# Optimization experiments

Measured on AMD Instinct MI355X. Metric: run time of the kernel, lower is better.

Reference implementation:

```python
import jax, jax.numpy as jnp
import numpy as np

EPS = 1e-08

def _householder(x, v):
    # x: [B,S,r], v: [B,S,r]; H x = x - 2 v_n (v_n . x), v_n = v/||v||
    v_norm_sq = jnp.sum(v * v, axis=-1, keepdims=True) + EPS
    v_n = v / jnp.sqrt(v_norm_sq)
    vTx = jnp.sum(x * v_n, axis=-1, keepdims=True)
    return x - 2.0 * v_n * vTx

def setup_inputs() -> dict:
    key = jax.random.key(0)
    ks = jax.random.split(key, 8)
    B, S, D, R = 4, 4096, 1024, 256
    N_IN, N_PROC, N_OUT, K = 16, 64, 16, 8
    x = jax.random.normal(ks[0], (B, S, D), dtype=jnp.float32)
    input_idx = jax.random.randint(ks[1], (B, S), 0, N_IN)
    process_indices = jax.random.randint(ks[2], (B, S, K), 0, N_PROC)
    output_idx = jax.random.randint(ks[3], (B, S), 0, N_OUT)
    # learned params (orthogonal-ish init approximated by scaled gaussian)
    input_neurons = jax.random.normal(ks[4], (N_IN, D, R), dtype=jnp.float32) / np.sqrt(D)
    pv = jax.random.normal(ks[5], (N_PROC, R), dtype=jnp.float32)
    process_neurons = pv / (jnp.linalg.norm(pv, axis=-1, keepdims=True) + EPS)
    output_neurons = jax.random.normal(ks[6], (N_OUT, R, D), dtype=jnp.float32) / np.sqrt(D)
    return {"x": x, "input_neurons": input_neurons, "process_neurons": process_neurons,
            "output_neurons": output_neurons, "input_idx": input_idx,
            "process_indices": process_indices, "output_idx": output_idx}

def reference(x, input_neurons, process_neurons, output_neurons,
              input_idx, process_indices, output_idx):
    # ---- input projection (hard selection): d_model -> rank ----
    # compute all-expert projections then gather per token (avoids [B,S,D,R] gather)
    all_in = jnp.einsum('bsd,ndr->bsnr', x, input_neurons)          # [B,S,n_in,R]
    h = jnp.take_along_axis(all_in, input_idx[..., None, None], axis=2)[:, :, 0, :]  # [B,S,R]
    # ---- process: k sequential Householder reflections ----
    selected_v = process_neurons[process_indices]                    # [B,S,k,R]
    vs = jnp.moveaxis(selected_v, 2, 0)                              # [k,B,S,R]
    def step(carry, v):
        return _householder(carry, v), None
    h, _ = jax.lax.scan(step, h, vs)
    # ---- output projection (hard selection): rank -> d_model ----
    all_out = jnp.einsum('bsr,nrd->bsnd', h, output_neurons)         # [B,S,n_out,D]
    out = jnp.take_along_axis(all_out, output_idx[..., None, None], axis=2)[:, :, 0, :]
    return out
```

## Files before the change

kernel.cpp:

```cpp
#include <hip/hip_runtime.h>
#include <hip/hip_bf16.h>

#define NT    16384
#define DM    1024
#define RK    256
#define N_IN  16
#define N_OUT 16
#define KHH   8
#define MAXTOK 1536
#define BM    64
#define TPE   (MAXTOK / BM)
#define KC    4

typedef short bf16x8 __attribute__((ext_vector_type(8)));
typedef float f32x4 __attribute__((ext_vector_type(4)));
typedef unsigned short u16;
typedef u16 u16x8 __attribute__((ext_vector_type(8)));
typedef u16 u16x4 __attribute__((ext_vector_type(4)));

__device__ __forceinline__ u16 f2bf(float f) {
  __hip_bfloat16 b = __float2bfloat16(f);
  return *reinterpret_cast<u16*>(&b);
}
__device__ __forceinline__ float bf2f(u16 u) {
  return __uint_as_float((unsigned)u << 16);
}

__device__ __forceinline__ void gl_lds16(const void* g, void* lds) {
  __builtin_amdgcn_global_load_lds(
      (const __attribute__((address_space(1))) void*)g,
      (__attribute__((address_space(3))) void*)lds, 16, 0, 0);
}

__global__ __launch_bounds__(256) void build_lists_pn(
    const int* __restrict__ in_idx, const int* __restrict__ out_idx,
    const float* __restrict__ pn,
    int* __restrict__ list_in, int* __restrict__ cnt_in,
    int* __restrict__ list_out, int* __restrict__ cnt_out,
    float* __restrict__ pnorm2) {
  const int b = blockIdx.x;
  const int tid = threadIdx.x, lane = tid & 63, wid = tid >> 6;

  if (b == 32) {
    const int p = tid >> 2, q = tid & 3;
    const float* row = pn + (size_t)p * RK + q * 64;
    float s = 0.f;
#pragma unroll
    for (int i = 0; i < 16; i++) {
      const float4 v = ((const float4*)row)[i];
      s += v.x * v.x + v.y * v.y + v.z * v.z + v.w * v.w;
    }
    s += __shfl_xor(s, 1);
    s += __shfl_xor(s, 2);
    if (q == 0) pnorm2[p] = s + 1e-8f;
    return;
  }

  const int e = b & 15, which = b >> 4;
  const int* __restrict__ idx = which ? out_idx : in_idx;
  int* __restrict__ list = (which ? list_out : list_in) + (size_t)e * NT;
  int* __restrict__ cnt = (which ? cnt_out : cnt_in) + e;

  __shared__ int wsum[4];
  const unsigned long long lt = (1ull << lane) - 1ull;
  int off = 0;
  for (int base = 0; base < NT; base += 1024) {
    const int4 iv = ((const int4*)(idx + base))[tid];
    const bool f0 = iv.x == e, f1 = iv.y == e, f2 = iv.z == e, f3 = iv.w == e;
    const unsigned long long m0 = __ballot(f0), m1 = __ballot(f1),
                             m2 = __ballot(f2), m3 = __ballot(f3);
    const int below = __popcll(m0 & lt) + __popcll(m1 & lt) +
                      __popcll(m2 & lt) + __popcll(m3 & lt);
    const int wtot = __popcll(m0) + __popcll(m1) + __popcll(m2) + __popcll(m3);
    if (lane == 0) wsum[wid] = wtot;
    __syncthreads();
    int b0 = 0, tot = 0;
#pragma unroll
    for (int w = 0; w < 4; w++) { if (w < wid) b0 += wsum[w]; tot += wsum[w]; }
    int pos = off + b0 + below;
    const int t = base + tid * 4;
    if (f0) list[pos++] = t;
    if (f1) list[pos++] = t + 1;
    if (f2) list[pos++] = t + 2;
    if (f3) list[pos++] = t + 3;
    off += tot;
    __syncthreads();
  }
  if (tid == 0) *cnt = off;
}

__global__ __launch_bounds__(256) void transpose_cvt2(
    const float* __restrict__ Win, const float* __restrict__ Wout,
    u16* __restrict__ WinT, u16* __restrict__ WoT) {
  const int z = blockIdx.z;
  const float* __restrict__ src = z ? Wout : Win;
  u16* __restrict__ dst = z ? WoT : WinT;
  const int R = z ? RK : DM, C = z ? DM : RK;
  const int e = blockIdx.y;
  const int tilesC = C >> 6;
  const int tr = (blockIdx.x / tilesC) << 6;
  const int tc = (blockIdx.x % tilesC) << 6;
  __shared__ float ls[64][65];
  const int t = threadIdx.x;
  const int row = t >> 2, q = t & 3;
  const float* s = src + (size_t)e * R * C + (size_t)(tr + row) * C + tc + q * 16;
#pragma unroll
  for (int j = 0; j < 4; j++) {
    const float4 v = ((const float4*)s)[j];
    ls[row][q * 16 + j * 4 + 0] = v.x;
    ls[row][q * 16 + j * 4 + 1] = v.y;
    ls[row][q * 16 + j * 4 + 2] = v.z;
    ls[row][q * 16 + j * 4 + 3] = v.w;
  }
  __syncthreads();
  const int cc = t >> 2;
  u16x8 o0, o1;
#pragma unroll
  for (int j = 0; j < 8; j++) o0[j] = f2bf(ls[q * 16 + j][cc]);
#pragma unroll
  for (int j = 0; j < 8; j++) o1[j] = f2bf(ls[q * 16 + 8 + j][cc]);
  u16* d = dst + (size_t)e * C * R + (size_t)(tc + cc) * R + tr + q * 16;
  ((u16x8*)d)[0] = o0;
  ((u16x8*)d)[1] = o1;
}

__global__ __launch_bounds__(256, 4) void input_gemm_part(
    const float* __restrict__ x, const u16* __restrict__ WinT,
    const int* __restrict__ list, const int* __restrict__ cnt,
    u16* __restrict__ h4) {
  const int bid = blockIdx.x;
  const int xcd = bid & 7;
  int j = bid >> 3;
  const int tile = j % TPE;
  j /= TPE;
  const int nb = j & 1;
  const int e = xcd * 2 + ((j >> 1) & 1);
  const int kc = j >> 2;
  const int nt = cnt[e];
  const int t0 = tile * BM;
  if (t0 >= nt) return;
  const int* __restrict__ lst = list + (size_t)e * NT + t0;
  const int ntok = min(BM, nt - t0);

  __shared__ __align__(16) u16 As[BM * 64];
  __shared__ __align__(16) u16 Bs[128 * 64];
  __shared__ int toks[BM];

  const int tid = threadIdx.x, lane = tid & 63, w = tid >> 6;
  if (tid < BM) toks[tid] = lst[tid < ntok ? tid : 0];
  __syncthreads();

  const int arow = tid >> 3, k8 = tid & 7;
  const float* axp0 = x + (size_t)toks[arow] * DM + kc * 256 + k8 * 8;
  const float* axp1 = x + (size_t)toks[arow + 32] * DM + kc * 256 + k8 * 8;
  const int aoff0 = arow * 128 + ((k8 ^ (arow & 7)) << 4);
  const int aoff1 = (arow + 32) * 128 + ((k8 ^ (arow & 7)) << 4);

  const int sub = lane >> 3;
  const int swz8 = ((lane & 7) ^ sub) * 8;
  const u16* Wbase = WinT + (size_t)e * RK * DM + (size_t)(nb * 128) * DM + kc * 256;

  f32x4 acc[4][2];
#pragma unroll
  for (int m = 0; m < 4; m++)
#pragma unroll
    for (int jx = 0; jx < 2; jx++) acc[m][jx] = (f32x4)0.f;

  const int l15 = lane & 15, lg = lane >> 4;

  float4 af[2][2][2];
#pragma unroll
  for (int p = 0; p < 2; ++p) {
    af[p][0][0] = ((const float4*)(axp0 + p * 64))[0];
    af[p][0][1] = ((const float4*)(axp0 + p * 64))[1];
    af[p][1][0] = ((const float4*)(axp1 + p * 64))[0];
    af[p][1][1] = ((const float4*)(axp1 + p * 64))[1];
  }

#pragma unroll
  for (int it = 0; it < 4; ++it) {
    const int s = it & 1;
    const int k0 = it * 64;
    if (it) __syncthreads();
    u16x8 a0, a1;
    a0[0] = f2bf(af[s][0][0].x); a0[1] = f2bf(af[s][0][0].y);
    a0[2] = f2bf(af[s][0][0].z); a0[3] = f2bf(af[s][0][0].w);
    a0[4] = f2bf(af[s][0][1].x); a0[5] = f2bf(af[s][0][1].y);
    a0[6] = f2bf(af[s][0][1].z); a0[7] = f2bf(af[s][0][1].w);
    a1[0] = f2bf(af[s][1][0].x); a1[1] = f2bf(af[s][1][0].y);
    a1[2] = f2bf(af[s][1][0].z); a1[3] = f2bf(af[s][1][0].w);
    a1[4] = f2bf(af[s][1][1].x); a1[5] = f2bf(af[s][1][1].y);
    a1[6] = f2bf(af[s][1][1].z); a1[7] = f2bf(af[s][1][1].w);
    if (it + 2 < 4) {
      af[s][0][0] = ((const float4*)(axp0 + (it + 2) * 64))[0];
      af[s][0][1] = ((const float4*)(axp0 + (it + 2) * 64))[1];
      af[s][1][0] = ((const float4*)(axp1 + (it + 2) * 64))[0];
      af[s][1][1] = ((const float4*)(axp1 + (it + 2) * 64))[1];
    }
#pragma unroll
    for (int i = 0; i < 4; ++i) {
      const int g = w * 4 + i;
      const int n = g * 8 + sub;
      gl_lds16(Wbase + (size_t)n * DM + k0 + swz8, Bs + g * 512);
    }
    *(u16x8*)((char*)As + aoff0) = a0;
    *(u16x8*)((char*)As + aoff1) = a1;
    __syncthreads();
#pragma unroll
    for (int kk = 0; kk < 2; ++kk) {
      const int sw = (((kk * 4 + lg) ^ (l15 & 7)) << 4);
      bf16x8 fa[4];
#pragma unroll
      for (int m = 0; m < 4; ++m)
        fa[m] = *(const bf16x8*)((const char*)As + (m * 16 + l15) * 128 + sw);
#pragma unroll
      for (int jx = 0; jx < 2; ++jx) {
        const int n = w * 32 + jx * 16 + l15;
        const bf16x8 fb = *(const bf16x8*)((const char*)Bs + n * 128 + sw);
#pragma unroll
        for (int m = 0; m < 4; ++m)
          acc[m][jx] = __builtin_amdgcn_mfma_f32_16x16x32_bf16(fa[m], fb, acc[m][jx], 0, 0, 0);
      }
    }
  }

  u16* hp4 = h4 + (size_t)kc * NT * RK;
#pragma unroll
  for (int m = 0; m < 4; ++m)
#pragma unroll
    for (int r = 0; r < 4; ++r) {
      const int slot = m * 16 + lg * 4 + r;
      if (slot < ntok) {
        u16* hp = hp4 + (size_t)toks[slot] * RK + nb * 128 + w * 32 + l15;
#pragma unroll
        for (int jx = 0; jx < 2; ++jx) hp[jx * 16] = f2bf(acc[m][jx][r]);
      }
    }
}

__global__ __launch_bounds__(256) void hh_k(
    const u16* __restrict__ h4, u16* __restrict__ hb,
    const float* __restrict__ pn, const float* __restrict__ pnorm2,
    const int* __restrict__ pidx) {
  const int lane = threadIdx.x & 63;
  const int t = blockIdx.x * 4 + (threadIdx.x >> 6);

  float4 hv;
  {
    const u16x4 p0 = ((const u16x4*)(h4 + ((size_t)0 * NT + t) * RK))[lane];
    const u16x4 p1 = ((const u16x4*)(h4 + ((size_t)1 * NT + t) * RK))[lane];
    const u16x4 p2 = ((const u16x4*)(h4 + ((size_t)2 * NT + t) * RK))[lane];
    const u16x4 p3 = ((const u16x4*)(h4 + ((size_t)3 * NT + t) * RK))[lane];
    hv.x = (bf2f(p0[0]) + bf2f(p1[0])) + (bf2f(p2[0]) + bf2f(p3[0]));
    hv.y = (bf2f(p0[1]) + bf2f(p1[1])) + (bf2f(p2[1]) + bf2f(p3[1]));
    hv.z = (bf2f(p0[2]) + bf2f(p1[2])) + (bf2f(p2[2]) + bf2f(p3[2]));
    hv.w = (bf2f(p0[3]) + bf2f(p1[3])) + (bf2f(p2[3]) + bf2f(p3[3]));
  }

#pragma unroll
  for (int k = 0; k < KHH; k++) {
    const int p = pidx[t * KHH + k];
    const float4 v = ((const float4*)(pn + (size_t)p * RK))[lane];
    float dvh = v.x * hv.x + v.y * hv.y + v.z * hv.z + v.w * hv.w;
#pragma unroll
    for (int s = 32; s; s >>= 1) dvh += __shfl_xor(dvh, s);
    const float c = 2.f * dvh / pnorm2[p];
    hv.x = fmaf(-c, v.x, hv.x);
    hv.y = fmaf(-c, v.y, hv.y);
    hv.z = fmaf(-c, v.z, hv.z);
    hv.w = fmaf(-c, v.w, hv.w);
  }
  u16x4 o;
  o[0] = f2bf(hv.x); o[1] = f2bf(hv.y); o[2] = f2bf(hv.z); o[3] = f2bf(hv.w);
  ((u16x4*)(hb + (size_t)t * RK))[lane] = o;
}

__global__ __launch_bounds__(256, 6) void output_gemm_mfma(
    const u16* __restrict__ hb, const u16* __restrict__ WoT,
    const int* __restrict__ list, const int* __restrict__ cnt,
    float* __restrict__ out) {
  const int bid = blockIdx.x;
  const int xcd = bid & 7;
  int j = bid >> 3;
  const int tile = j % TPE;
  j /= TPE;
  const int e = xcd * 2 + (j & 1);
  const int cb = j >> 1;
  const int nt = cnt[e];
  const int t0 = tile * BM;
  if (t0 >= nt) return;
  const int* __restrict__ lst = list + (size_t)e * NT + t0;
  const int ntok = min(BM, nt - t0);

  __shared__ __align__(16) u16 As[BM * 64];
  __shared__ __align__(16) u16 Bs[128 * 64];
  __shared__ int toks[BM];

  const int tid = threadIdx.x, lane = tid & 63, w = tid >> 6;
  if (tid < BM) toks[tid] = lst[tid < ntok ? tid : 0];
  __syncthreads();

  const int sub = lane >> 3;
  const int swz8 = ((lane & 7) ^ sub) * 8;
  const u16* Wbase = WoT + (size_t)e * DM * RK + (size_t)(cb * 128) * RK;
  const int ar0 = (w * 2 + 0) * 8 + sub;
  const int ar1 = (w * 2 + 1) * 8 + sub;
  const u16* asrc0 = hb + (size_t)toks[ar0] * RK + swz8;
  const u16* asrc1 = hb + (size_t)toks[ar1] * RK + swz8;

  f32x4 acc[4][2];
#pragma unroll
  for (int m = 0; m < 4; m++)
#pragma unroll
    for (int jx = 0; jx < 2; jx++) acc[m][jx] = (f32x4)0.f;

  const int l15 = lane & 15, lg = lane >> 4;

#pragma unroll
  for (int it = 0; it < RK / 64; ++it) {
    const int k0 = it * 64;
    if (it) __syncthreads();
    gl_lds16(asrc0 + k0, As + (w * 2 + 0) * 512);
    gl_lds16(asrc1 + k0, As + (w * 2 + 1) * 512);
#pragma unroll
    for (int i = 0; i < 4; ++i) {
      const int g = w * 4 + i;
      const int n = g * 8 + sub;
      gl_lds16(Wbase + (size_t)n * RK + k0 + swz8, Bs + g * 512);
    }
    __syncthreads();
#pragma unroll
    for (int kk = 0; kk < 2; ++kk) {
      const int sw = (((kk * 4 + lg) ^ (l15 & 7)) << 4);
      bf16x8 fa[4];
#pragma unroll
      for (int m = 0; m < 4; ++m)
        fa[m] = *(const bf16x8*)((const char*)As + (m * 16 + l15) * 128 + sw);
#pragma unroll
      for (int jx = 0; jx < 2; ++jx) {
        const int n = w * 32 + jx * 16 + l15;
        const bf16x8 fb = *(const bf16x8*)((const char*)Bs + n * 128 + sw);
#pragma unroll
        for (int m = 0; m < 4; ++m)
          acc[m][jx] = __builtin_amdgcn_mfma_f32_16x16x32_bf16(fa[m], fb, acc[m][jx], 0, 0, 0);
      }
    }
  }

#pragma unroll
  for (int m = 0; m < 4; ++m)
#pragma unroll
    for (int r = 0; r < 4; ++r) {
      const int slot = m * 16 + lg * 4 + r;
      if (slot < ntok) {
        float* op = out + (size_t)toks[slot] * DM + cb * 128 + w * 32 + l15;
#pragma unroll
        for (int jx = 0; jx < 2; ++jx) op[jx * 16] = acc[m][jx][r];
      }
    }
}

extern "C" void kernel_launch(void* const* d_in, const int* in_sizes, int n_in,
                              void* d_out, int out_size, void* d_ws,
                              size_t ws_size, hipStream_t stream) {
  const float* x     = (const float*)d_in[0];
  const float* Win   = (const float*)d_in[1];
  const float* pn    = (const float*)d_in[2];
  const float* Wout  = (const float*)d_in[3];
  const int* in_idx  = (const int*)d_in[4];
  const int* pidx    = (const int*)d_in[5];
  const int* out_idx = (const int*)d_in[6];
  float* out = (float*)d_out;

  char* ws = (char*)d_ws;
  u16* WinT  = (u16*)ws;                    ws += (size_t)N_IN * RK * DM * 2;
  u16* WoT   = (u16*)ws;                    ws += (size_t)N_OUT * DM * RK * 2;
  u16* hb    = (u16*)ws;                    ws += (size_t)NT * RK * 2;
  u16* h4    = (u16*)ws;                    ws += (size_t)KC * NT * RK * 2;
  int* list_in  = (int*)ws;                 ws += (size_t)N_IN * NT * 4;
  int* list_out = (int*)ws;                 ws += (size_t)N_OUT * NT * 4;
  int* cnt_in   = (int*)ws;                 ws += 64;
  int* cnt_out  = (int*)ws;                 ws += 64;
  float* pnorm2 = (float*)ws;

  hipLaunchKernelGGL(build_lists_pn, dim3(33), dim3(256), 0, stream,
                     in_idx, out_idx, pn, list_in, cnt_in, list_out, cnt_out,
                     pnorm2);
  hipLaunchKernelGGL(transpose_cvt2, dim3(64, 16, 2), dim3(256), 0, stream,
                     Win, Wout, WinT, WoT);
  hipLaunchKernelGGL(input_gemm_part, dim3(8 * TPE * 16), dim3(256), 0,
                     stream, x, WinT, list_in, cnt_in, h4);
  hipLaunchKernelGGL(hh_k, dim3(NT / 4), dim3(256), 0, stream,
                     h4, hb, pn, pnorm2, pidx);
  hipLaunchKernelGGL(output_gemm_mfma, dim3(8 * TPE * 16), dim3(256), 0,
                     stream, hb, WoT, list_out, cnt_out, out);
}
```

Measured before the change: 84.43 us.

## Fold weight transposes into list-building and input GEMM kernels to cut launches

Removes the standalone transpose kernel. The Win transpose now runs as extra blocks of the list-building kernel, and the Wout transpose runs as extra blocks appended to the input GEMM grid, sharing a union shared-memory buffer. This drops one kernel launch and its serialization, letting independent work overlap with the list building and GEMM. The cost is a larger static shared allocation for the list kernel (64x65 floats) and more blocks in the GEMM grid, which may affect occupancy and scheduling.

```diff
diff --git a/kernel.cpp b/kernel.cpp
--- a/kernel.cpp
+++ b/kernel.cpp
@@ -11,6 +11,8 @@
 #define BM    64
 #define TPE   (MAXTOK / BM)
 #define KC    4
+#define GEMM_BLKS (8 * TPE * 16)
+#define TWOUT_BLKS (16 * 64)
 
 typedef short bf16x8 __attribute__((ext_vector_type(8)));
 typedef float f32x4 __attribute__((ext_vector_type(4)));
@@ -32,15 +34,50 @@
       (__attribute__((address_space(3))) void*)lds, 16, 0, 0);
 }
 
-__global__ __launch_bounds__(256) void build_lists_pn(
+__device__ __forceinline__ void transpose_tile(
+    const float* __restrict__ src, u16* __restrict__ dst,
+    int R, int C, int e, int tile, float (*ls)[65], int t) {
+  const int tilesC = C >> 6;
+  const int tr = (tile / tilesC) << 6;
+  const int tc = (tile % tilesC) << 6;
+  const int row = t >> 2, q = t & 3;
+  const float* s = src + (size_t)e * R * C + (size_t)(tr + row) * C + tc + q * 16;
+#pragma unroll
+  for (int j = 0; j < 4; j++) {
+    const float4 v = ((const float4*)s)[j];
+    ls[row][q * 16 + j * 4 + 0] = v.x;
+    ls[row][q * 16 + j * 4 + 1] = v.y;
+    ls[row][q * 16 + j * 4 + 2] = v.z;
+    ls[row][q * 16 + j * 4 + 3] = v.w;
+  }
+  __syncthreads();
+  const int cc = t >> 2;
+  u16x8 o0, o1;
+#pragma unroll
+  for (int j = 0; j < 8; j++) o0[j] = f2bf(ls[q * 16 + j][cc]);
+#pragma unroll
+  for (int j = 0; j < 8; j++) o1[j] = f2bf(ls[q * 16 + 8 + j][cc]);
+  u16* d = dst + (size_t)e * C * R + (size_t)(tc + cc) * R + tr + q * 16;
+  ((u16x8*)d)[0] = o0;
+  ((u16x8*)d)[1] = o1;
+}
+
+__global__ __launch_bounds__(256) void lists_pn_winT(
     const int* __restrict__ in_idx, const int* __restrict__ out_idx,
-    const float* __restrict__ pn,
+    const float* __restrict__ pn, const float* __restrict__ Win,
     int* __restrict__ list_in, int* __restrict__ cnt_in,
     int* __restrict__ list_out, int* __restrict__ cnt_out,
-    float* __restrict__ pnorm2) {
+    float* __restrict__ pnorm2, u16* __restrict__ WinT) {
   const int b = blockIdx.x;
   const int tid = threadIdx.x, lane = tid & 63, wid = tid >> 6;
-
+  __shared__ float ls[64][65];
+  __shared__ int wsum[4];
+
+  if (b >= 33) {
+    const int b2 = b - 33;
+    transpose_tile(Win, WinT, DM, RK, b2 >> 6, b2 & 63, ls, tid);
+    return;
+  }
   if (b == 32) {
     const int p = tid >> 2, q = tid & 3;
     const float* row = pn + (size_t)p * RK + q * 64;
@@ -61,7 +98,6 @@
   int* __restrict__ list = (which ? list_out : list_in) + (size_t)e * NT;
   int* __restrict__ cnt = (which ? cnt_out : cnt_in) + e;
 
-  __shared__ int wsum[4];
   const unsigned long long lt = (1ull << lane) - 1ull;
   int off = 0;
   for (int base = 0; base < NT; base += 1024) {
@@ -89,46 +125,22 @@
   if (tid == 0) *cnt = off;
 }
 
-__global__ __launch_bounds__(256) void transpose_cvt2(
-    const float* __restrict__ Win, const float* __restrict__ Wout,
-    u16* __restrict__ WinT, u16* __restrict__ WoT) {
-  const int z = blockIdx.z;
-  const float* __restrict__ src = z ? Wout : Win;
-  u16* __restrict__ dst = z ? WoT : WinT;
-  const int R = z ? RK : DM, C = z ? DM : RK;
-  const int e = blockIdx.y;
-  const int tilesC = C >> 6;
-  const int tr = (blockIdx.x / tilesC) << 6;
-  const int tc = (blockIdx.x % tilesC) << 6;
-  __shared__ float ls[64][65];
-  const int t = threadIdx.x;
-  const int row = t >> 2, q = t & 3;
-  const float* s = src + (size_t)e * R * C + (size_t)(tr + row) * C + tc + q * 16;
-#pragma unroll
-  for (int j = 0; j < 4; j++) {
-    const float4 v = ((const float4*)s)[j];
-    ls[row][q * 16 + j * 4 + 0] = v.x;
-    ls[row][q * 16 + j * 4 + 1] = v.y;
-    ls[row][q * 16 + j * 4 + 2] = v.z;
-    ls[row][q * 16 + j * 4 + 3] = v.w;
-  }
-  __syncthreads();
-  const int cc = t >> 2;
-  u16x8 o0, o1;
-#pragma unroll
-  for (int j = 0; j < 8; j++) o0[j] = f2bf(ls[q * 16 + j][cc]);
-#pragma unroll
-  for (int j = 0; j < 8; j++) o1[j] = f2bf(ls[q * 16 + 8 + j][cc]);
-  u16* d = dst + (size_t)e * C * R + (size_t)(tc + cc) * R + tr + q * 16;
-  ((u16x8*)d)[0] = o0;
-  ((u16x8*)d)[1] = o1;
-}
-
-__global__ __launch_bounds__(256, 4) void input_gemm_part(
+__global__ __launch_bounds__(256, 4) void input_gemm_woT(
     const float* __restrict__ x, const u16* __restrict__ WinT,
     const int* __restrict__ list, const int* __restrict__ cnt,
-    u16* __restrict__ h4) {
+    u16* __restrict__ h4,
+    const float* __restrict__ Wout, u16* __restrict__ WoT) {
+  __shared__ __align__(16) char smem[24832];
+  const int tid = threadIdx.x, lane = tid & 63, w = tid >> 6;
   const int bid = blockIdx.x;
+
+  if (bid >= GEMM_BLKS) {
+    const int b2 = bid - GEMM_BLKS;
+    transpose_tile(Wout, WoT, RK, DM, b2 >> 6, b2 & 63,
+                   (float(*)[65])smem, tid);
+    return;
+  }
+
   const int xcd = bid & 7;
   int j = bid >> 3;
   const int tile = j % TPE;
@@ -142,11 +154,10 @@
   const int* __restrict__ lst = list + (size_t)e * NT + t0;
   const int ntok = min(BM, nt - t0);
 
-  __shared__ __align__(16) u16 As[BM * 64];
-  __shared__ __align__(16) u16 Bs[128 * 64];
-  __shared__ int toks[BM];
-
-  const int tid = threadIdx.x, lane = tid & 63, w = tid >> 6;
+  u16* As = (u16*)smem;
+  u16* Bs = (u16*)(smem + 8192);
+  int* toks = (int*)(smem + 8192 + 16384);
+
   if (tid < BM) toks[tid] = lst[tid < ntok ? tid : 0];
   __syncthreads();
 
@@ -383,15 +394,13 @@
   int* cnt_out  = (int*)ws;                 ws += 64;
   float* pnorm2 = (float*)ws;
 
-  hipLaunchKernelGGL(build_lists_pn, dim3(33), dim3(256), 0, stream,
-                     in_idx, out_idx, pn, list_in, cnt_in, list_out, cnt_out,
-                     pnorm2);
-  hipLaunchKernelGGL(transpose_cvt2, dim3(64, 16, 2), dim3(256), 0, stream,
-                     Win, Wout, WinT, WoT);
-  hipLaunchKernelGGL(input_gemm_part, dim3(8 * TPE * 16), dim3(256), 0,
-                     stream, x, WinT, list_in, cnt_in, h4);
+  hipLaunchKernelGGL(lists_pn_winT, dim3(33 + 1024), dim3(256), 0, stream,
+                     in_idx, out_idx, pn, Win, list_in, cnt_in,
+                     list_out, cnt_out, pnorm2, WinT);
+  hipLaunchKernelGGL(input_gemm_woT, dim3(GEMM_BLKS + TWOUT_BLKS), dim3(256),
+                     0, stream, x, WinT, list_in, cnt_in, h4, Wout, WoT);
   hipLaunchKernelGGL(hh_k, dim3(NT / 4), dim3(256), 0, stream,
                      h4, hb, pn, pnorm2, pidx);
-  hipLaunchKernelGGL(output_gemm_mfma, dim3(8 * TPE * 16), dim3(256), 0,
-                     stream, hb, WoT, list_out, cnt_out, out);
-}
+  hipLaunchKernelGGL(output_gemm_mfma, dim3(GEMM_BLKS), dim3(256), 0, stream,
+                     hb, WoT, list_out, cnt_out, out);
+}
```

New measurement: 79.97 us. 5.3% less time.
